# Kernel tuning notes

Hardware: AMD Instinct MI355X
Metric: run time of the kernel (lower is better)

The kernel has to match this reference:

```python
import jax, jax.numpy as jnp
import numpy as np

IN_F = 4096
OUT_F = 4096
NNZ = 1638400
TOKENS = 8192


def setup_inputs() -> dict:
    key = jax.random.key(0)
    k1, k2, k3, k4, k5 = jax.random.split(key, 5)
    x = jax.random.normal(k1, (TOKENS, IN_F), dtype=jnp.float32)
    weight_pruned = jax.random.normal(k2, (NNZ,), dtype=jnp.float32)
    bias = jax.random.normal(k3, (OUT_F,), dtype=jnp.float32)
    row_idx = jax.random.randint(k4, (NNZ,), 0, OUT_F, dtype=jnp.int32)
    col_idx = jax.random.randint(k5, (NNZ,), 0, IN_F, dtype=jnp.int32)
    return {"x": x, "weight_pruned": weight_pruned, "bias": bias,
            "row_idx": row_idx, "col_idx": col_idx}


def reference(x, weight_pruned, bias, row_idx, col_idx):
    # matching torch advanced-index assignment), then dense linear.
    W = jnp.zeros((OUT_F, IN_F), dtype=weight_pruned.dtype)
    W = W.at[row_idx, col_idx].set(weight_pruned)
    return x @ W.T + bias
```

## Files before the change

kernel.cpp:

```cpp
#include <hip/hip_runtime.h>
#include <hip/hip_bf16.h>
#include <cstdint>

#define TOKENS 8192
#define IN_F 4096
#define OUT_F 4096

typedef __bf16 bf16x8 __attribute__((ext_vector_type(8)));
typedef float f32x4 __attribute__((ext_vector_type(4)));

__global__ void scatter_pack_kernel(const int* __restrict__ row,
                                    const int* __restrict__ col,
                                    const float* __restrict__ w,
                                    unsigned long long* __restrict__ P,
                                    int nnz) {
    int i = blockIdx.x * blockDim.x + threadIdx.x;
    if (i < nnz) {
        __bf16 b = (__bf16)w[i];
        unsigned short bits;
        __builtin_memcpy(&bits, &b, 2);
        unsigned long long pack =
            ((unsigned long long)(unsigned)i << 16) | (unsigned long long)bits;
        atomicMax(&P[(size_t)row[i] * IN_F + col[i]], pack);
    }
}

__global__ void extract_convert_kernel(const unsigned long long* __restrict__ P,
                                       __bf16* __restrict__ Wb,
                                       const float* __restrict__ x,
                                       __bf16* __restrict__ xb,
                                       int eb) {
    if ((int)blockIdx.x < eb) {
        size_t base = ((size_t)blockIdx.x * 256 + threadIdx.x) * 8;
        bf16x8 o;
#pragma unroll
        for (int j = 0; j < 8; ++j) {
            unsigned short bits = (unsigned short)(P[base + j] & 0xFFFFull);
            __bf16 b;
            __builtin_memcpy(&b, &bits, 2);
            o[j] = b;
        }
        *(bf16x8*)(Wb + base) = o;
    } else {
        size_t base = ((size_t)(blockIdx.x - eb) * 256 + threadIdx.x) * 8;
        float4 v0 = *(const float4*)(x + base);
        float4 v1 = *(const float4*)(x + base + 4);
        bf16x8 o;
        o[0] = (__bf16)v0.x; o[1] = (__bf16)v0.y;
        o[2] = (__bf16)v0.z; o[3] = (__bf16)v0.w;
        o[4] = (__bf16)v1.x; o[5] = (__bf16)v1.y;
        o[6] = (__bf16)v1.z; o[7] = (__bf16)v1.w;
        *(bf16x8*)(xb + base) = o;
    }
}

__global__ __launch_bounds__(256) void gemm_bt_kernel(
    const __bf16* __restrict__ A,
    const __bf16* __restrict__ B,
    const float* __restrict__ bias,
    float* __restrict__ C) {
    __shared__ __bf16 As[128 * 32];
    __shared__ __bf16 Bs[128 * 32];

    const int tid  = threadIdx.x;
    const int lane = tid & 63;
    const int wid  = tid >> 6;
    const int m0 = blockIdx.y * 128;
    const int n0 = blockIdx.x * 128;
    const int wm = (wid >> 1) * 64;
    const int wn = (wid & 1) * 64;

    const int srow = lane >> 2;
    const int scol = (lane & 3) * 8;
    const int c0 = wid * 2, c1 = wid * 2 + 1;

    const __bf16* ga0 = A + (size_t)(m0 + c0 * 16 + srow) * IN_F + scol;
    const __bf16* ga1 = A + (size_t)(m0 + c1 * 16 + srow) * IN_F + scol;
    const __bf16* gb0 = B + (size_t)(n0 + c0 * 16 + srow) * IN_F + scol;
    const __bf16* gb1 = B + (size_t)(n0 + c1 * 16 + srow) * IN_F + scol;

    __bf16* la0 = &As[c0 * 512];
    __bf16* la1 = &As[c1 * 512];
    __bf16* lb0 = &Bs[c0 * 512];
    __bf16* lb1 = &Bs[c1 * 512];

    const int fm = lane & 15;
    const int fq = (lane >> 4) * 8;
    const __bf16* fa = &As[(wm + fm) * 32 + fq];
    const __bf16* fb = &Bs[(wn + fm) * 32 + fq];

    f32x4 acc[4][4] = {};

    for (int kt = 0; kt < IN_F; kt += 32) {
        __builtin_amdgcn_global_load_lds(
            (unsigned int __attribute__((address_space(1)))*)(ga0 + kt),
            (unsigned int __attribute__((address_space(3)))*)la0, 16, 0, 0);
        __builtin_amdgcn_global_load_lds(
            (unsigned int __attribute__((address_space(1)))*)(ga1 + kt),
            (unsigned int __attribute__((address_space(3)))*)la1, 16, 0, 0);
        __builtin_amdgcn_global_load_lds(
            (unsigned int __attribute__((address_space(1)))*)(gb0 + kt),
            (unsigned int __attribute__((address_space(3)))*)lb0, 16, 0, 0);
        __builtin_amdgcn_global_load_lds(
            (unsigned int __attribute__((address_space(1)))*)(gb1 + kt),
            (unsigned int __attribute__((address_space(3)))*)lb1, 16, 0, 0);

        __syncthreads();

        bf16x8 afrag[4], bfrag[4];
#pragma unroll
        for (int t = 0; t < 4; ++t) afrag[t] = *(const bf16x8*)(fa + t * 512);
#pragma unroll
        for (int t = 0; t < 4; ++t) bfrag[t] = *(const bf16x8*)(fb + t * 512);

#pragma unroll
        for (int mt = 0; mt < 4; ++mt)
#pragma unroll
            for (int nt = 0; nt < 4; ++nt)
                acc[mt][nt] = __builtin_amdgcn_mfma_f32_16x16x32_bf16(
                    afrag[mt], bfrag[nt], acc[mt][nt], 0, 0, 0);

        __syncthreads();
    }

    float bv[4];
#pragma unroll
    for (int nt = 0; nt < 4; ++nt) bv[nt] = bias[n0 + wn + nt * 16 + fm];
    const int r0 = m0 + wm + (lane >> 4) * 4;
#pragma unroll
    for (int mt = 0; mt < 4; ++mt)
#pragma unroll
        for (int nt = 0; nt < 4; ++nt) {
            const int cc = n0 + wn + nt * 16 + fm;
#pragma unroll
            for (int i = 0; i < 4; ++i) {
                C[(size_t)(r0 + mt * 16 + i) * OUT_F + cc] = acc[mt][nt][i] + bv[nt];
            }
        }
}

extern "C" void kernel_launch(void* const* d_in, const int* in_sizes, int n_in,
                              void* d_out, int out_size, void* d_ws, size_t ws_size,
                              hipStream_t stream) {
    const float* x    = (const float*)d_in[0];
    const float* w    = (const float*)d_in[1];
    const float* bias = (const float*)d_in[2];
    const int*   row  = (const int*)d_in[3];
    const int*   col  = (const int*)d_in[4];
    float* out = (float*)d_out;
    const int nnz = in_sizes[3];

    __bf16* xb = (__bf16*)d_ws;
    __bf16* Wb = (__bf16*)((char*)d_ws + (size_t)TOKENS * IN_F * 2);
    unsigned long long* P = (unsigned long long*)d_out;

    hipMemsetAsync(P, 0, (size_t)OUT_F * IN_F * 8, stream);

    scatter_pack_kernel<<<(nnz + 255) / 256, 256, 0, stream>>>(row, col, w, P, nnz);

    const int eb = OUT_F * IN_F / (256 * 8);
    const int cb = TOKENS * IN_F / (256 * 8);
    extract_convert_kernel<<<eb + cb, 256, 0, stream>>>(P, Wb, x, xb, eb);

    dim3 grid(OUT_F / 128, TOKENS / 128);
    gemm_bt_kernel<<<grid, 256, 0, stream>>>(xb, Wb, bias, out);
}
```

Baseline: 634.1 us.

## Scatter 32-bit winning indices and XOR-swizzle GEMM LDS tiles

The scatter now records only the winning nonzero index with a 32-bit atomicMax into a map preset to -1, halving the memset and scatter footprint compared with 64-bit packed values. The extract pass then gathers the fp32 weight by index and converts it to bf16. Separately, the GEMM applies an XOR swizzle to the 16-byte chunk column on both the global-to-LDS store and the fragment reads to reduce LDS bank conflicts. The cost is an indirect, uncoalesced gather of w during extraction.

```diff
diff --git a/kernel.cpp b/kernel.cpp
--- a/kernel.cpp
+++ b/kernel.cpp
@@ -9,36 +9,30 @@
 typedef __bf16 bf16x8 __attribute__((ext_vector_type(8)));
 typedef float f32x4 __attribute__((ext_vector_type(4)));
 
-__global__ void scatter_pack_kernel(const int* __restrict__ row,
-                                    const int* __restrict__ col,
-                                    const float* __restrict__ w,
-                                    unsigned long long* __restrict__ P,
-                                    int nnz) {
+__global__ void scatter_max_kernel(const int* __restrict__ row,
+                                   const int* __restrict__ col,
+                                   int* __restrict__ M, int nnz) {
     int i = blockIdx.x * blockDim.x + threadIdx.x;
     if (i < nnz) {
-        __bf16 b = (__bf16)w[i];
-        unsigned short bits;
-        __builtin_memcpy(&bits, &b, 2);
-        unsigned long long pack =
-            ((unsigned long long)(unsigned)i << 16) | (unsigned long long)bits;
-        atomicMax(&P[(size_t)row[i] * IN_F + col[i]], pack);
+        atomicMax(&M[(size_t)row[i] * IN_F + col[i]], i);
     }
 }
 
-__global__ void extract_convert_kernel(const unsigned long long* __restrict__ P,
+__global__ void extract_convert_kernel(const int* __restrict__ M,
+                                       const float* __restrict__ w,
                                        __bf16* __restrict__ Wb,
                                        const float* __restrict__ x,
                                        __bf16* __restrict__ xb,
                                        int eb) {
     if ((int)blockIdx.x < eb) {
         size_t base = ((size_t)blockIdx.x * 256 + threadIdx.x) * 8;
+        int4 m0 = *(const int4*)(M + base);
+        int4 m1 = *(const int4*)(M + base + 4);
+        int idx[8] = {m0.x, m0.y, m0.z, m0.w, m1.x, m1.y, m1.z, m1.w};
         bf16x8 o;
 #pragma unroll
         for (int j = 0; j < 8; ++j) {
-            unsigned short bits = (unsigned short)(P[base + j] & 0xFFFFull);
-            __bf16 b;
-            __builtin_memcpy(&b, &bits, 2);
-            o[j] = b;
+            o[j] = (idx[j] >= 0) ? (__bf16)w[idx[j]] : (__bf16)0.0f;
         }
         *(bf16x8*)(Wb + base) = o;
     } else {
@@ -71,7 +65,7 @@
     const int wn = (wid & 1) * 64;
 
     const int srow = lane >> 2;
-    const int scol = (lane & 3) * 8;
+    const int scol = (((lane & 3) ^ ((lane >> 3) & 3)) * 8);
     const int c0 = wid * 2, c1 = wid * 2 + 1;
 
     const __bf16* ga0 = A + (size_t)(m0 + c0 * 16 + srow) * IN_F + scol;
@@ -85,9 +79,9 @@
     __bf16* lb1 = &Bs[c1 * 512];
 
     const int fm = lane & 15;
-    const int fq = (lane >> 4) * 8;
-    const __bf16* fa = &As[(wm + fm) * 32 + fq];
-    const __bf16* fb = &Bs[(wn + fm) * 32 + fq];
+    const int fc = (((lane >> 4) ^ ((fm >> 1) & 3)) * 8);
+    const __bf16* fa = &As[(wm + fm) * 32 + fc];
+    const __bf16* fb = &Bs[(wn + fm) * 32 + fc];
 
     f32x4 acc[4][4] = {};
 
@@ -152,15 +146,15 @@
 
     __bf16* xb = (__bf16*)d_ws;
     __bf16* Wb = (__bf16*)((char*)d_ws + (size_t)TOKENS * IN_F * 2);
-    unsigned long long* P = (unsigned long long*)d_out;
+    int* M = (int*)d_out;
 
-    hipMemsetAsync(P, 0, (size_t)OUT_F * IN_F * 8, stream);
+    hipMemsetAsync(M, 0xFF, (size_t)OUT_F * IN_F * 4, stream);
 
-    scatter_pack_kernel<<<(nnz + 255) / 256, 256, 0, stream>>>(row, col, w, P, nnz);
+    scatter_max_kernel<<<(nnz + 255) / 256, 256, 0, stream>>>(row, col, M, nnz);
 
     const int eb = OUT_F * IN_F / (256 * 8);
     const int cb = TOKENS * IN_F / (256 * 8);
-    extract_convert_kernel<<<eb + cb, 256, 0, stream>>>(P, Wb, x, xb, eb);
+    extract_convert_kernel<<<eb + cb, 256, 0, stream>>>(M, w, Wb, x, xb, eb);
 
     dim3 grid(OUT_F / 128, TOKENS / 128);
     gemm_bt_kernel<<<grid, 256, 0, stream>>>(xb, Wb, bias, out);
```

After: 624.2 us. Within noise of the previous version (-1.6%).
